# Optimization experiments

Measured on AMD Instinct MI355X. Metric: run time of the kernel, lower is better.

The kernel has to match this reference:

```python
import jax, jax.numpy as jnp
import numpy as np

NEURON_CDECAY = 0.5
NEURON_VDECAY = 0.75
NEURON_VTH = 0.5
PSEUDO_WINDOW = 0.5

@jax.custom_vjp
def pseudo_spike(v):
    return (v > NEURON_VTH).astype(v.dtype)

def _ps_fwd(v):
    return pseudo_spike(v), v

def _ps_bwd(v, g):
    return (g * (jnp.abs(v - NEURON_VTH) < PSEUDO_WINDOW).astype(g.dtype),)

pseudo_spike.defvjp(_ps_fwd, _ps_bwd)

def clif_scan(X_tbd):
    # X_tbd: [T, B, D] synaptic inputs; CLIF neuron recurrence over time.
    def step(carry, x_t):
        c, v, s = carry
        c = c * NEURON_CDECAY + x_t
        v = v * NEURON_VDECAY * (1.0 - s) + c
        s = pseudo_spike(v)
        return (c, v, s), s
    z = jnp.zeros(X_tbd.shape[1:], X_tbd.dtype)
    _, spikes = jax.lax.scan(step, (z, z, z), X_tbd)
    return spikes  # [T, B, D]

def setup_inputs() -> dict:
    key = jax.random.key(0)
    ks = jax.random.split(key, 8)
    B, IN, H1, H2, OUT, T = 256, 2048, 2048, 2048, 1024, 16
    def lin(k, fan_in, fan_out):
        bound = 1.0 / np.sqrt(fan_in)
        kw, kb = jax.random.split(k)
        W = jax.random.uniform(kw, (fan_out, fan_in), jnp.float32, -bound, bound)
        b = jax.random.uniform(kb, (fan_out,), jnp.float32, -bound, bound)
        return W, b
    W0, b0 = lin(ks[0], IN, H1)
    W1, b1 = lin(ks[1], H1, H2)
    W_out, b_out = lin(ks[2], H2, OUT)
    in_pop_spikes = (jax.random.uniform(ks[3], (B, IN, T), jnp.float32) < 0.5).astype(jnp.float32)
    return {"in_pop_spikes": in_pop_spikes, "W0": W0, "b0": b0, "W1": W1, "b1": b1,
            "W_out": W_out, "b_out": b_out, "batch_size": B, "update": 0, "re_calibration": 0}

def reference(in_pop_spikes, W0, b0, W1, b1, W_out, b_out, batch_size, update, re_calibration):
    # layer 0: linear over all timesteps, then CLIF scan
    x = jnp.moveaxis(in_pop_spikes, -1, 0)                    # [T, B, IN]
    s0 = clif_scan(jnp.einsum('tbi,hi->tbh', x, W0) + b0)     # [T, B, H1]
    s1 = clif_scan(jnp.einsum('tbh,gh->tbg', s0, W1) + b1)    # [T, B, H2]
    so = clif_scan(jnp.einsum('tbg,og->tbo', s1, W_out) + b_out)  # [T, B, OUT]
    return jnp.mean(so, axis=0)  # out_pop_act: sum over T / spike_ts
```

## Files before the change

### kernel.cpp

```cpp
#include <hip/hip_runtime.h>
#include <stdint.h>


typedef int v4i __attribute__((ext_vector_type(4)));
typedef int v16i __attribute__((ext_vector_type(16)));

#define TT 16
constexpr int KD = 2048;
constexpr double SCALE = 68719476736.0;

#define GLOAD_LDS16(g, s)                                                      \
  __builtin_amdgcn_global_load_lds(                                            \
      (const __attribute__((address_space(1))) uint32_t*)(g),                  \
      (__attribute__((address_space(3))) uint32_t*)(s), 16, 0, 0)

__device__ __forceinline__ size_t af_addr(int m, int k) {
  return ((size_t)((m >> 5) * 64 + (k >> 5)) << 10)
       + ((size_t)((m & 31) + (((k >> 4) & 1) << 5)) << 4) + (k & 15);
}

__global__ __launch_bounds__(256)
void prep_limbs_wf(const float* __restrict__ W, int8_t* __restrict__ dst,
                   int total ) {
  const int g = blockIdx.x * 256 + threadIdx.x;
  const int lane = g & 63;
  const int n = ((g >> 12) << 5) + (lane & 31);
  const int k0 = (((g & 4095) >> 6) << 5) + ((lane >> 5) << 4);
  const float* src = W + (size_t)n * 2048 + k0;
  float4 wv[4];
#pragma unroll
  for (int q = 0; q < 4; ++q) wv[q] = *reinterpret_cast<const float4*>(src + q * 4);
  const float* f = reinterpret_cast<const float*>(wv);
  long long nn[16];
#pragma unroll
  for (int e = 0; e < 16; ++e) nn[e] = (long long)rint((double)f[e] * SCALE);
  const size_t base = (size_t)g * 16;
#pragma unroll
  for (int l = 0; l < 4; ++l) {
    alignas(16) char c[16];
#pragma unroll
    for (int e = 0; e < 16; ++e) {
      const int d = (int)((nn[e] + 128) & 255) - 128;
      c[e] = (char)d;
      nn[e] = (nn[e] - d) >> 8;
    }
    *reinterpret_cast<v4i*>(dst + (size_t)l * total + base) = *(const v4i*)c;
  }
}

__global__ __launch_bounds__(256)
void transpose_x_af(const float* __restrict__ in, int8_t* __restrict__ out) {
  const int idx = blockIdx.x * 256 + threadIdx.x;
  const float4* src = reinterpret_cast<const float4*>(in) + (size_t)idx * 4;
  float4 v[4];
  v[0] = src[0]; v[1] = src[1]; v[2] = src[2]; v[3] = src[3];
  const float* f = reinterpret_cast<const float*>(v);
  const int b = idx >> 11, i = idx & 2047;
  const size_t base = af_addr(b * TT, i);
#pragma unroll
  for (int t = 0; t < TT; ++t) out[base + (size_t)t * 16] = (int8_t)f[t];
}

static __device__ __forceinline__ v16i zero16() {
  v16i z;
#pragma unroll
  for (int i = 0; i < 16; ++i) z[i] = 0;
  return z;
}

template<int N, bool FINAL>
__global__ __launch_bounds__(256, 2)
void gemm_scan_i8(const int8_t* __restrict__ AF,
                  const int8_t* __restrict__ WF,
                  const float* __restrict__ bias,
                  void* __restrict__ outp) {
  __shared__ union SM {
    int8_t buf[3][24 * 1024];
    double c[4][32 * 33];
  } sm;

  const int tid = threadIdx.x;
  const int lane = tid & 63;
  const int w = tid >> 6;
  const int wy = w >> 1, nsub = w & 1;
  const int m0 = blockIdx.x * 128;
  const int n0 = blockIdx.y * 64;
  const size_t lst = (size_t)N * KD;

  const int8_t* asrc[2];
  int adst[2];
#pragma unroll
  for (int j = 0; j < 2; ++j) {
    const int fa = w + 4 * j;
    asrc[j] = AF + ((size_t)(((m0 >> 5) + (fa >> 1)) * 64 + (fa & 1)) << 10)
            + lane * 16;
    adst[j] = fa * 1024;
  }
  const int8_t* bsrc[4];
  int bdst[4];
#pragma unroll
  for (int j = 0; j < 4; ++j) {
    const int f = w + 4 * j;
    const int l = f >> 2, kk = (f >> 1) & 1, ns = f & 1;
    bsrc[j] = WF + (size_t)l * lst
            + ((size_t)(((n0 >> 5) + ns) * 64 + kk) << 10) + lane * 16;
    bdst[j] = (8 + f) * 1024;
  }

#define STAGE(T, BUF)                                                          \
  {                                                                            \
    _Pragma("unroll")                                                          \
    for (int j = 0; j < 2; ++j)                                                \
      GLOAD_LDS16(asrc[j] + (size_t)(T) * 2048, &sm.buf[BUF][adst[j]]);        \
    _Pragma("unroll")                                                          \
    for (int j = 0; j < 4; ++j)                                                \
      GLOAD_LDS16(bsrc[j] + (size_t)(T) * 2048, &sm.buf[BUF][bdst[j]]);        \
  }

  v16i acc[4][2];
#pragma unroll
  for (int l = 0; l < 4; ++l) { acc[l][0] = zero16(); acc[l][1] = zero16(); }

  constexpr int NT2 = KD / 64;

  STAGE(0, 0);
  STAGE(1, 1);

  int bufc = 0;
  for (int t2 = 0; t2 < NT2; ++t2) {
    if (t2 == NT2 - 1) asm volatile("s_waitcnt vmcnt(0)" ::: "memory");
    else               asm volatile("s_waitcnt vmcnt(6)" ::: "memory");
    __builtin_amdgcn_s_barrier();
    if (t2 + 2 < NT2) {
      int b2 = bufc + 2; if (b2 >= 3) b2 -= 3;
      STAGE(t2 + 2, b2);
    }
    const int8_t* bb = sm.buf[bufc];
    v4i afr[2][2];
#pragma unroll
    for (int mi = 0; mi < 2; ++mi)
#pragma unroll
      for (int kk = 0; kk < 2; ++kk)
        afr[mi][kk] = *(const v4i*)(bb + ((((wy * 2 + mi) << 1) | kk) << 10)
                                       + lane * 16);
    __builtin_amdgcn_s_setprio(1);
#pragma unroll
    for (int l = 0; l < 4; ++l)
#pragma unroll
      for (int kk = 0; kk < 2; ++kk) {
        const v4i bf = *(const v4i*)(bb + ((8 + ((l << 2) | (kk << 1) | nsub)) << 10)
                                        + lane * 16);
        acc[l][0] = __builtin_amdgcn_mfma_i32_32x32x32_i8(afr[0][kk], bf, acc[l][0], 0, 0, 0);
        acc[l][1] = __builtin_amdgcn_mfma_i32_32x32x32_i8(afr[1][kk], bf, acc[l][1], 0, 0, 0);
      }
    __builtin_amdgcn_s_setprio(0);
    ++bufc; if (bufc == 3) bufc = 0;
  }
#undef STAGE

  const int rep = (lane & 31) * 0x01010101;
  v4i rowv; rowv[0] = rep; rowv[1] = rep; rowv[2] = rep; rowv[3] = rep;
  v4i onev; onev[0] = 0x01010101; onev[1] = 0x01010101;
            onev[2] = 0x01010101; onev[3] = 0x01010101;
  const v16i drow = __builtin_amdgcn_mfma_i32_32x32x32_i8(rowv, onev, zero16(), 0, 0, 0);
  const v16i dcol = __builtin_amdgcn_mfma_i32_32x32x32_i8(onev, rowv, zero16(), 0, 0, 0);

  const int col = lane & 31;
  const int bl = lane >> 5;
  double* cw = sm.c[w];
#pragma unroll
  for (int mi = 0; mi < 2; ++mi) {
    __syncthreads();
#pragma unroll
    for (int i = 0; i < 16; ++i) {
      long long ts = acc[3][mi][i];
      ts = (ts << 8) + acc[2][mi][i];
      ts = (ts << 8) + acc[1][mi][i];
      ts = (ts << 8) + acc[0][mi][i];
      cw[(drow[i] >> 5) * 33 + (dcol[i] >> 5)] = (double)ts * 0x1p-36;
    }
    __syncthreads();

    const int gn = n0 + nsub * 32 + col;
    const int gm = m0 + (wy * 2 + mi) * 32 + bl * 16;
    const double bj = (double)bias[gn];
    double cc = 0.0, vv = 0.0, ss = 0.0;
    if (!FINAL) {
      int8_t* so = (int8_t*)outp;
      const size_t ab = af_addr(gm, gn);
#pragma unroll
      for (int t = 0; t < TT; ++t) {
        const double x = cw[(bl * 16 + t) * 33 + col] + bj;
        cc = cc * 0.5 + x;
        vv = vv * 0.75 * (1.0 - ss) + cc;
        ss = (vv > 0.5) ? 1.0 : 0.0;
        so[ab + (size_t)t * 16] = (int8_t)ss;
      }
    } else {
      float tot = 0.0f;
#pragma unroll
      for (int t = 0; t < TT; ++t) {
        const double x = cw[(bl * 16 + t) * 33 + col] + bj;
        cc = cc * 0.5 + x;
        vv = vv * 0.75 * (1.0 - ss) + cc;
        ss = (vv > 0.5) ? 1.0 : 0.0;
        tot += (float)ss;
      }
      ((float*)outp)[(size_t)(gm / TT) * N + gn] = tot * 0.0625f;
    }
  }
}

extern "C" void kernel_launch(void* const* d_in, const int* in_sizes, int n_in,
                              void* d_out, int out_size, void* d_ws, size_t ws_size,
                              hipStream_t stream) {
  const float* X  = (const float*)d_in[0];
  const float* W0 = (const float*)d_in[1];
  const float* b0 = (const float*)d_in[2];
  const float* W1 = (const float*)d_in[3];
  const float* b1 = (const float*)d_in[4];
  const float* Wo = (const float*)d_in[5];
  const float* bo = (const float*)d_in[6];
  float* out = (float*)d_out;

  int8_t* base = (int8_t*)d_ws;
  int8_t* AF0 = base;
  int8_t* AF1 = base + (size_t)8388608;
  int8_t* AF2 = AF0;
  int8_t* F0  = base + (size_t)16777216;
  int8_t* F1  = base + (size_t)33554432;
  int8_t* Fo  = base + (size_t)50331648;

  prep_limbs_wf<<<1024, 256, 0, stream>>>(W0, F0, 2048 * 2048);
  prep_limbs_wf<<<1024, 256, 0, stream>>>(W1, F1, 2048 * 2048);
  prep_limbs_wf<<< 512, 256, 0, stream>>>(Wo, Fo, 1024 * 2048);
  transpose_x_af<<<2048, 256, 0, stream>>>(X, AF0);

  gemm_scan_i8<2048, false><<<dim3(32, 32), 256, 0, stream>>>(AF0, F0, b0, AF1);
  gemm_scan_i8<2048, false><<<dim3(32, 32), 256, 0, stream>>>(AF1, F1, b1, AF2);
  gemm_scan_i8<1024, true ><<<dim3(32, 16), 256, 0, stream>>>(AF2, Fo, bo, out);
}
```

Measured before the change: 198.3 us.

## Swizzle workgroup order across XCDs and split LDS fragment loads into two phases

Launches the GEMM-scan kernel on a 1D grid and remaps block IDs so that consecutive blocks on each XCD (round-robin by h&7) cover 8x8 panels of M/N tiles. The intent is better L2 reuse of shared A and B tiles. The inner loop now loads B fragments in two halves with explicit barriers, lgkmcnt waits and sched_barriers between the MFMA groups, so LDS reads and MFMAs are interleaved across waves. The added s_barriers per iteration could cost synchronization overhead.

```diff
diff --git a/kernel.cpp b/kernel.cpp
--- a/kernel.cpp
+++ b/kernel.cpp
@@ -83,8 +83,17 @@
   const int lane = tid & 63;
   const int w = tid >> 6;
   const int wy = w >> 1, nsub = w & 1;
-  const int m0 = blockIdx.x * 128;
-  const int n0 = blockIdx.y * 64;
+
+  constexpr int NN = N / 64;
+  constexpr int NWG = 32 * NN;
+  const int h = blockIdx.x;
+  const int wk = (h & 7) * (NWG >> 3) + (h >> 3);
+  const int panel = wk >> 6;
+  const int within = wk & 63;
+  const int mt = (panel & 3) * 8 + (within & 7);
+  const int nt = (panel >> 2) * 8 + (within >> 3);
+  const int m0 = mt * 128;
+  const int n0 = nt * 64;
   const size_t lst = (size_t)N * KD;
 
   const int8_t* asrc[2];
@@ -136,24 +145,53 @@
       STAGE(t2 + 2, b2);
     }
     const int8_t* bb = sm.buf[bufc];
-    v4i afr[2][2];
+
+    v4i afr[2][2], b01[2][2];
 #pragma unroll
     for (int mi = 0; mi < 2; ++mi)
 #pragma unroll
       for (int kk = 0; kk < 2; ++kk)
         afr[mi][kk] = *(const v4i*)(bb + ((((wy * 2 + mi) << 1) | kk) << 10)
                                        + lane * 16);
+#pragma unroll
+    for (int l = 0; l < 2; ++l)
+#pragma unroll
+      for (int kk = 0; kk < 2; ++kk)
+        b01[l][kk] = *(const v4i*)(bb + ((8 + ((l << 2) | (kk << 1) | nsub)) << 10)
+                                      + lane * 16);
+    __builtin_amdgcn_s_barrier();
+    asm volatile("s_waitcnt lgkmcnt(0)" ::: "memory");
+    __builtin_amdgcn_sched_barrier(0);
     __builtin_amdgcn_s_setprio(1);
 #pragma unroll
-    for (int l = 0; l < 4; ++l)
+    for (int l = 0; l < 2; ++l)
 #pragma unroll
       for (int kk = 0; kk < 2; ++kk) {
-        const v4i bf = *(const v4i*)(bb + ((8 + ((l << 2) | (kk << 1) | nsub)) << 10)
-                                        + lane * 16);
-        acc[l][0] = __builtin_amdgcn_mfma_i32_32x32x32_i8(afr[0][kk], bf, acc[l][0], 0, 0, 0);
-        acc[l][1] = __builtin_amdgcn_mfma_i32_32x32x32_i8(afr[1][kk], bf, acc[l][1], 0, 0, 0);
+        acc[l][0] = __builtin_amdgcn_mfma_i32_32x32x32_i8(afr[0][kk], b01[l][kk], acc[l][0], 0, 0, 0);
+        acc[l][1] = __builtin_amdgcn_mfma_i32_32x32x32_i8(afr[1][kk], b01[l][kk], acc[l][1], 0, 0, 0);
       }
     __builtin_amdgcn_s_setprio(0);
+
+    v4i b23[2][2];
+#pragma unroll
+    for (int l = 0; l < 2; ++l)
+#pragma unroll
+      for (int kk = 0; kk < 2; ++kk)
+        b23[l][kk] = *(const v4i*)(bb + ((8 + (((l + 2) << 2) | (kk << 1) | nsub)) << 10)
+                                      + lane * 16);
+    __builtin_amdgcn_s_barrier();
+    asm volatile("s_waitcnt lgkmcnt(0)" ::: "memory");
+    __builtin_amdgcn_sched_barrier(0);
+    __builtin_amdgcn_s_setprio(1);
+#pragma unroll
+    for (int l = 0; l < 2; ++l)
+#pragma unroll
+      for (int kk = 0; kk < 2; ++kk) {
+        acc[l + 2][0] = __builtin_amdgcn_mfma_i32_32x32x32_i8(afr[0][kk], b23[l][kk], acc[l + 2][0], 0, 0, 0);
+        acc[l + 2][1] = __builtin_amdgcn_mfma_i32_32x32x32_i8(afr[1][kk], b23[l][kk], acc[l + 2][1], 0, 0, 0);
+      }
+    __builtin_amdgcn_s_setprio(0);
+
     ++bufc; if (bufc == 3) bufc = 0;
   }
 #undef STAGE
@@ -236,7 +274,7 @@
   prep_limbs_wf<<< 512, 256, 0, stream>>>(Wo, Fo, 1024 * 2048);
   transpose_x_af<<<2048, 256, 0, stream>>>(X, AF0);
 
-  gemm_scan_i8<2048, false><<<dim3(32, 32), 256, 0, stream>>>(AF0, F0, b0, AF1);
-  gemm_scan_i8<2048, false><<<dim3(32, 32), 256, 0, stream>>>(AF1, F1, b1, AF2);
-  gemm_scan_i8<1024, true ><<<dim3(32, 16), 256, 0, stream>>>(AF2, Fo, bo, out);
-}
+  gemm_scan_i8<2048, false><<<1024, 256, 0, stream>>>(AF0, F0, b0, AF1);
+  gemm_scan_i8<2048, false><<<1024, 256, 0, stream>>>(AF1, F1, b1, AF2);
+  gemm_scan_i8<1024, true ><<< 512, 256, 0, stream>>>(AF2, Fo, bo, out);
+}
```

Measured after the change: 192.9 us. 2.7% less time.

## Interleave staged loads with MFMA groups, swizzle tiles for L2, fuse weight prep

Applied to the files above, without the earlier changes.

The global-to-LDS prefetch for the next-next K tile is now split into chunks and interleaved with four groups of MFMAs, each group gated by a barrier and an LDS wait. The goal is to spread memory issue across the compute loop. The GEMM grid becomes 1D with an XCD-aware remap into 8x8 tile panels, meant to improve L2 reuse of A and B across workgroups. The three weight-limb prep launches are merged into one kernel to cut launch overhead. The extra barriers per K step add synchronisation cost that could offset the gains.

```diff
diff --git a/kernel.cpp b/kernel.cpp
--- a/kernel.cpp
+++ b/kernel.cpp
@@ -20,9 +20,17 @@
 }
 
 __global__ __launch_bounds__(256)
-void prep_limbs_wf(const float* __restrict__ W, int8_t* __restrict__ dst,
-                   int total ) {
-  const int g = blockIdx.x * 256 + threadIdx.x;
+void prep_limbs_all(const float* __restrict__ W0, const float* __restrict__ W1,
+                    const float* __restrict__ Wo, int8_t* __restrict__ F0,
+                    int8_t* __restrict__ F1, int8_t* __restrict__ Fo) {
+  int blk = blockIdx.x;
+  const float* W;
+  int8_t* dst;
+  int total;
+  if (blk < 1024)      { W = W0; dst = F0; total = 2048 * 2048; }
+  else if (blk < 2048) { W = W1; dst = F1; total = 2048 * 2048; blk -= 1024; }
+  else                 { W = Wo; dst = Fo; total = 1024 * 2048; blk -= 2048; }
+  const int g = blk * 256 + threadIdx.x;
   const int lane = g & 63;
   const int n = ((g >> 12) << 5) + (lane & 31);
   const int k0 = (((g & 4095) >> 6) << 5) + ((lane >> 5) << 4);
@@ -83,8 +91,17 @@
   const int lane = tid & 63;
   const int w = tid >> 6;
   const int wy = w >> 1, nsub = w & 1;
-  const int m0 = blockIdx.x * 128;
-  const int n0 = blockIdx.y * 64;
+
+  constexpr int NN = N / 64;
+  constexpr int NWG = 32 * NN;
+  const int h = blockIdx.x;
+  const int wk = (h & 7) * (NWG >> 3) + (h >> 3);
+  const int panel = wk >> 6;
+  const int within = wk & 63;
+  const int mt = (panel & 3) * 8 + (within & 7);
+  const int nt = (panel >> 2) * 8 + (within >> 3);
+  const int m0 = mt * 128;
+  const int n0 = nt * 64;
   const size_t lst = (size_t)N * KD;
 
   const int8_t* asrc[2];
@@ -107,56 +124,88 @@
     bdst[j] = (8 + f) * 1024;
   }
 
-#define STAGE(T, BUF)                                                          \
-  {                                                                            \
-    _Pragma("unroll")                                                          \
-    for (int j = 0; j < 2; ++j)                                                \
-      GLOAD_LDS16(asrc[j] + (size_t)(T) * 2048, &sm.buf[BUF][adst[j]]);        \
-    _Pragma("unroll")                                                          \
-    for (int j = 0; j < 4; ++j)                                                \
-      GLOAD_LDS16(bsrc[j] + (size_t)(T) * 2048, &sm.buf[BUF][bdst[j]]);        \
-  }
-
   v16i acc[4][2];
 #pragma unroll
   for (int l = 0; l < 4; ++l) { acc[l][0] = zero16(); acc[l][1] = zero16(); }
 
   constexpr int NT2 = KD / 64;
 
-  STAGE(0, 0);
-  STAGE(1, 1);
+#pragma unroll
+  for (int j = 0; j < 2; ++j) GLOAD_LDS16(asrc[j], &sm.buf[0][adst[j]]);
+#pragma unroll
+  for (int j = 0; j < 4; ++j) GLOAD_LDS16(bsrc[j], &sm.buf[0][bdst[j]]);
+#pragma unroll
+  for (int j = 0; j < 2; ++j) GLOAD_LDS16(asrc[j] + 2048, &sm.buf[1][adst[j]]);
+#pragma unroll
+  for (int j = 0; j < 4; ++j) GLOAD_LDS16(bsrc[j] + 2048, &sm.buf[1][bdst[j]]);
+
+#define GATE()                                                                 \
+  __builtin_amdgcn_s_barrier();                                                \
+  asm volatile("s_waitcnt lgkmcnt(0)" ::: "memory");                           \
+  __builtin_amdgcn_sched_barrier(0)
+
+#define MFMA4(L, BF)                                                           \
+  __builtin_amdgcn_s_setprio(1);                                               \
+  acc[L][0] = __builtin_amdgcn_mfma_i32_32x32x32_i8(afr[0][0], BF[0], acc[L][0], 0, 0, 0); \
+  acc[L][1] = __builtin_amdgcn_mfma_i32_32x32x32_i8(afr[1][0], BF[0], acc[L][1], 0, 0, 0); \
+  acc[L][0] = __builtin_amdgcn_mfma_i32_32x32x32_i8(afr[0][1], BF[1], acc[L][0], 0, 0, 0); \
+  acc[L][1] = __builtin_amdgcn_mfma_i32_32x32x32_i8(afr[1][1], BF[1], acc[L][1], 0, 0, 0); \
+  __builtin_amdgcn_s_setprio(0)
+
+#define BREAD(BF, L)                                                           \
+  BF[0] = *(const v4i*)(bb + ((8 + (((L) << 2) | nsub)) << 10) + lane * 16);   \
+  BF[1] = *(const v4i*)(bb + ((8 + (((L) << 2) | 2 | nsub)) << 10) + lane * 16)
 
   int bufc = 0;
   for (int t2 = 0; t2 < NT2; ++t2) {
     if (t2 == NT2 - 1) asm volatile("s_waitcnt vmcnt(0)" ::: "memory");
     else               asm volatile("s_waitcnt vmcnt(6)" ::: "memory");
     __builtin_amdgcn_s_barrier();
-    if (t2 + 2 < NT2) {
-      int b2 = bufc + 2; if (b2 >= 3) b2 -= 3;
-      STAGE(t2 + 2, b2);
-    }
     const int8_t* bb = sm.buf[bufc];
-    v4i afr[2][2];
+    int b2 = bufc + 2; if (b2 >= 3) b2 -= 3;
+    const bool stage = (t2 + 2 < NT2);
+    const size_t soff = (size_t)(t2 + 2) * 2048;
+
+    v4i afr[2][2], bf0[2], bf1[2];
+    if (stage) {
+      GLOAD_LDS16(asrc[0] + soff, &sm.buf[b2][adst[0]]);
+      GLOAD_LDS16(asrc[1] + soff, &sm.buf[b2][adst[1]]);
+    }
 #pragma unroll
     for (int mi = 0; mi < 2; ++mi)
 #pragma unroll
       for (int kk = 0; kk < 2; ++kk)
         afr[mi][kk] = *(const v4i*)(bb + ((((wy * 2 + mi) << 1) | kk) << 10)
                                        + lane * 16);
-    __builtin_amdgcn_s_setprio(1);
-#pragma unroll
-    for (int l = 0; l < 4; ++l)
-#pragma unroll
-      for (int kk = 0; kk < 2; ++kk) {
-        const v4i bf = *(const v4i*)(bb + ((8 + ((l << 2) | (kk << 1) | nsub)) << 10)
-                                        + lane * 16);
-        acc[l][0] = __builtin_amdgcn_mfma_i32_32x32x32_i8(afr[0][kk], bf, acc[l][0], 0, 0, 0);
-        acc[l][1] = __builtin_amdgcn_mfma_i32_32x32x32_i8(afr[1][kk], bf, acc[l][1], 0, 0, 0);
-      }
-    __builtin_amdgcn_s_setprio(0);
+    BREAD(bf0, 0);
+    GATE();
+    MFMA4(0, bf0);
+
+    if (stage) {
+      GLOAD_LDS16(bsrc[0] + soff, &sm.buf[b2][bdst[0]]);
+      GLOAD_LDS16(bsrc[1] + soff, &sm.buf[b2][bdst[1]]);
+    }
+    BREAD(bf1, 1);
+    GATE();
+    MFMA4(1, bf1);
+
+    if (stage) {
+      GLOAD_LDS16(bsrc[2] + soff, &sm.buf[b2][bdst[2]]);
+      GLOAD_LDS16(bsrc[3] + soff, &sm.buf[b2][bdst[3]]);
+    }
+    BREAD(bf0, 2);
+    GATE();
+    MFMA4(2, bf0);
+
+    BREAD(bf1, 3);
+    GATE();
+    MFMA4(3, bf1);
+
     ++bufc; if (bufc == 3) bufc = 0;
   }
-#undef STAGE
+#undef BREAD
+#undef MFMA4
+#undef GATE
 
   const int rep = (lane & 31) * 0x01010101;
   v4i rowv; rowv[0] = rep; rowv[1] = rep; rowv[2] = rep; rowv[3] = rep;
@@ -231,12 +280,10 @@
   int8_t* F1  = base + (size_t)33554432;
   int8_t* Fo  = base + (size_t)50331648;
 
-  prep_limbs_wf<<<1024, 256, 0, stream>>>(W0, F0, 2048 * 2048);
-  prep_limbs_wf<<<1024, 256, 0, stream>>>(W1, F1, 2048 * 2048);
-  prep_limbs_wf<<< 512, 256, 0, stream>>>(Wo, Fo, 1024 * 2048);
+  prep_limbs_all<<<2560, 256, 0, stream>>>(W0, W1, Wo, F0, F1, Fo);
   transpose_x_af<<<2048, 256, 0, stream>>>(X, AF0);
 
-  gemm_scan_i8<2048, false><<<dim3(32, 32), 256, 0, stream>>>(AF0, F0, b0, AF1);
-  gemm_scan_i8<2048, false><<<dim3(32, 32), 256, 0, stream>>>(AF1, F1, b1, AF2);
-  gemm_scan_i8<1024, true ><<<dim3(32, 16), 256, 0, stream>>>(AF2, Fo, bo, out);
-}
+  gemm_scan_i8<2048, false><<<1024, 256, 0, stream>>>(AF0, F0, b0, AF1);
+  gemm_scan_i8<2048, false><<<1024, 256, 0, stream>>>(AF1, F1, b1, AF2);
+  gemm_scan_i8<1024, true ><<< 512, 256, 0, stream>>>(AF2, Fo, bo, out);
+}
```

After: 186.4 us. -6.0%, faster.
